# Performance work log

Measured on AMD Instinct MI355X. Metric: run time of the kernel, lower is better.

## Reference

```python
import jax, jax.numpy as jnp
import numpy as np

B, S, D = 2, 2048, 1024
H, KV, HD = 16, 4, 64
E, TOPK, F = 8, 2, 2048
EPS = 1e-5
THETA = 10000.0


def setup_inputs() -> dict:
    key = jax.random.key(0)
    ks = jax.random.split(key, 12)
    sc = 0.02
    x = jax.random.normal(ks[0], (B, S, D), jnp.float32)
    # real RoPE tables
    inv = 1.0 / (THETA ** (np.arange(0, HD, 2, dtype=np.float32) / HD))
    t = np.arange(S, dtype=np.float32)
    f = np.outer(t, inv)  # [S, HD/2]
    freqs_cos = jnp.asarray(np.cos(f), jnp.float32)
    freqs_sin = jnp.asarray(np.sin(f), jnp.float32)
    return {
        "x": x,
        "freqs_cos": freqs_cos,
        "freqs_sin": freqs_sin,
        "attn_norm_w": jnp.ones((D,), jnp.float32),
        "ffn_norm_w": jnp.ones((D,), jnp.float32),
        "wq": jax.random.normal(ks[1], (D, H * HD), jnp.float32) * sc,
        "wk": jax.random.normal(ks[2], (D, KV * HD), jnp.float32) * sc,
        "wv": jax.random.normal(ks[3], (D, KV * HD), jnp.float32) * sc,
        "wo": jax.random.normal(ks[4], (H * HD, D), jnp.float32) * sc,
        "gate_w": jax.random.normal(ks[5], (D, E), jnp.float32) * sc,
        "w1": jax.random.normal(ks[6], (E, D, F), jnp.float32) * sc,
        "w2": jax.random.normal(ks[7], (E, F, D), jnp.float32) * sc,
        "w3": jax.random.normal(ks[8], (E, D, F), jnp.float32) * sc,
    }


def rmsnorm(x, w):
    return x * jax.lax.rsqrt(jnp.mean(x * x, axis=-1, keepdims=True) + EPS) * w


def apply_rope(xq, cos, sin):
    # xq: [B,S,h,HD]; cos/sin: [S, HD/2]
    xr, xi = xq[..., 0::2], xq[..., 1::2]
    c = cos[None, :, None, :]
    s = sin[None, :, None, :]
    out = jnp.stack([xr * c - xi * s, xr * s + xi * c], axis=-1)
    return out.reshape(xq.shape)


def attention(xn, freqs_cos, freqs_sin, wq, wk, wv, wo):
    q = (xn @ wq).reshape(B, S, H, HD)
    k = (xn @ wk).reshape(B, S, KV, HD)
    v = (xn @ wv).reshape(B, S, KV, HD)
    q = apply_rope(q, freqs_cos, freqs_sin)
    k = apply_rope(k, freqs_cos, freqs_sin)
    n_rep = H // KV
    k = jnp.repeat(k, n_rep, axis=2)  # [B,S,H,HD]
    v = jnp.repeat(v, n_rep, axis=2)
    scores = jnp.einsum("bqhd,bkhd->bhqk", q, k) / jnp.sqrt(jnp.float32(HD))
    causal = jnp.tril(jnp.ones((S, S), bool))
    scores = jnp.where(causal[None, None], scores, jnp.finfo(scores.dtype).min)
    probs = jax.nn.softmax(scores, axis=-1)
    out = jnp.einsum("bhqk,bkhd->bqhd", probs, v).reshape(B, S, H * HD)
    return out @ wo


def sparse_moe(hn, gate_w, w1, w2, w3):
    xf = hn.reshape(-1, D)  # [T, D]
    probs = jax.nn.softmax(xf @ gate_w, axis=-1)  # [T, E]
    topv, topi = jax.lax.top_k(probs, TOPK)
    topv = topv / jnp.sum(topv, axis=-1, keepdims=True)
    # dense [T, E] routing weights (0 for non-selected experts)
    wdense = jnp.sum(jax.nn.one_hot(topi, E, dtype=xf.dtype) * topv[..., None], axis=1)
    h1 = jax.nn.silu(jnp.einsum("td,edf->etf", xf, w1))
    h3 = jnp.einsum("td,edf->etf", xf, w3)
    y = jnp.einsum("etf,efd->etd", h1 * h3, w2)
    out = jnp.einsum("te,etd->td", wdense, y)
    return out.reshape(B, S, D)


def reference(x, freqs_cos, freqs_sin, attn_norm_w, ffn_norm_w,
              wq, wk, wv, wo, gate_w, w1, w2, w3):
    h = x + attention(rmsnorm(x, attn_norm_w), freqs_cos, freqs_sin, wq, wk, wv, wo)
    out = h + sparse_moe(rmsnorm(h, ffn_norm_w), gate_w, w1, w2, w3)
    return out
```

## Files before the change

### kernel.cpp

```cpp
#include <hip/hip_runtime.h>
#include <stdint.h>

typedef unsigned short u16;
typedef unsigned int u32;
typedef __attribute__((ext_vector_type(8))) short short8;
typedef __attribute__((ext_vector_type(8))) u16 us8;
typedef __attribute__((ext_vector_type(4))) u16 us4;
typedef __attribute__((ext_vector_type(4))) float f32x4;

constexpr int NB = 2;
constexpr int SEQ = 2048;
constexpr int DIM = 1024;
constexpr int NH = 16;
constexpr int HD = 64;
constexpr int NE = 8;
constexpr int FF = 2048;
constexpr int TOK = NB * SEQ;
constexpr int NQKV = 1536;
constexpr int NPAIR = TOK * 2;
constexpr float REPS = 1e-5f;

#define VMCNT(n) asm volatile("s_waitcnt vmcnt(" #n ")" ::: "memory")
#define LGKM0 asm volatile("s_waitcnt lgkmcnt(0)" ::: "memory")

__device__ __forceinline__ u16 f2bf(float x) {
  union { float f; u32 u; } v; v.f = x;
  u32 r = v.u + 0x7fffu + ((v.u >> 16) & 1u);
  return (u16)(r >> 16);
}
__device__ __forceinline__ float bf2f(u16 h) {
  union { u32 u; float f; } v; v.u = ((u32)h) << 16;
  return v.f;
}

__device__ __forceinline__ void gl_lds16(const u16* g, u16* l) {
  __builtin_amdgcn_global_load_lds(
      (const __attribute__((address_space(1))) void*)g,
      (__attribute__((address_space(3))) void*)l, 16, 0, 0);
}

template <bool SPLIT>
__global__ __launch_bounds__(256) void tcvt_k(const float* __restrict__ src,
                                              u16* __restrict__ dhi,
                                              u16* __restrict__ dlo,
                                              int K, int N) {
  int z = blockIdx.z;
  src += (size_t)z * K * N;
  dhi += (size_t)z * K * N;
  if (SPLIT) dlo += (size_t)z * K * N;
  int n0 = blockIdx.x * 64, k0 = blockIdx.y * 64;
  __shared__ float tile[64][65];
  int t = threadIdx.x;
  int kk = t >> 4, nn4 = (t & 15) * 4;
#pragma unroll
  for (int i = 0; i < 4; i++) {
    int k = kk + i * 16;
    const float* p = src + (size_t)(k0 + k) * N + n0 + nn4;
    float4 v = *(const float4*)p;
    tile[nn4 + 0][k] = v.x;
    tile[nn4 + 1][k] = v.y;
    tile[nn4 + 2][k] = v.z;
    tile[nn4 + 3][k] = v.w;
  }
  __syncthreads();
  int nn = t >> 4, k4 = (t & 15) * 4;
#pragma unroll
  for (int i = 0; i < 4; i++) {
    int n = nn + i * 16;
    us4 hi, lo;
#pragma unroll
    for (int j = 0; j < 4; j++) {
      float f = tile[n][k4 + j];
      u16 h = f2bf(f);
      hi[j] = h;
      if (SPLIT) lo[j] = f2bf(f - bf2f(h));
    }
    *(us4*)(dhi + (size_t)(n0 + n) * K + k0 + k4) = hi;
    if (SPLIT) *(us4*)(dlo + (size_t)(n0 + n) * K + k0 + k4) = lo;
  }
}

template <bool SPLIT>
__global__ __launch_bounds__(256) void rmsnorm_k(const float* __restrict__ x,
                                                 const float* __restrict__ w,
                                                 u16* __restrict__ ohi,
                                                 u16* __restrict__ olo) {
  int row = blockIdx.x, t = threadIdx.x;
  float4 v = *(const float4*)(x + (size_t)row * DIM + t * 4);
  float ss = v.x * v.x + v.y * v.y + v.z * v.z + v.w * v.w;
#pragma unroll
  for (int m = 1; m < 64; m <<= 1) ss += __shfl_xor(ss, m);
  __shared__ float red[4];
  if ((t & 63) == 0) red[t >> 6] = ss;
  __syncthreads();
  float rstd = rsqrtf((red[0] + red[1] + red[2] + red[3]) * (1.0f / DIM) + REPS);
  float4 wv = *(const float4*)(w + t * 4);
  float os[4] = {v.x * rstd * wv.x, v.y * rstd * wv.y, v.z * rstd * wv.z,
                 v.w * rstd * wv.w};
  us4 hi, lo;
#pragma unroll
  for (int j = 0; j < 4; j++) {
    u16 h = f2bf(os[j]);
    hi[j] = h;
    if (SPLIT) lo[j] = f2bf(os[j] - bf2f(h));
  }
  *(us4*)(ohi + (size_t)row * DIM + t * 4) = hi;
  if (SPLIT) *(us4*)(olo + (size_t)row * DIM + t * 4) = lo;
}

template <int EPI, bool SPLIT, bool DUAL, bool PERSIST, int NXL, int NT>
__global__ __launch_bounds__(256, 2) void gemm_k(
    const u16* __restrict__ Ah, const u16* __restrict__ Al,
    const u16* __restrict__ Bh, const u16* __restrict__ Bl,
    const u16* __restrict__ B1, int N, int ldc,
    float* __restrict__ Cf, u16* __restrict__ Cb, float* __restrict__ C2,
    const float* __restrict__ resid, const int* __restrict__ cnt,
    const int* __restrict__ pids, const float* __restrict__ pw,
    const int* __restrict__ plan) {
  constexpr int K = NT * 32;
  constexpr int BN = SPLIT ? 64 : 128;
  constexpr int WCOL = BN / 2;
  constexpr int FN = BN / 32;
  constexpr int NAI = 2;
  constexpr int NBI = BN / 64;
  constexpr int BUFA = 128 * 32;
  constexpr int BUFB = BN * 32;
  constexpr bool L6 = SPLIT || DUAL;

  int tid = threadIdx.x, lane = tid & 63, wid = tid >> 6;
  int wm = wid >> 1, wn = wid & 1;
  int rr = lane & 15, g = lane >> 4;

  __shared__ u16 sAh[3 * BUFA];
  __shared__ u16 sAl[SPLIT ? 3 * BUFA : 16];
  __shared__ u16 sBh[3 * BUFB];
  __shared__ u16 sBl[SPLIT ? 3 * BUFB : 16];
  __shared__ u16 sB1[DUAL ? 3 * BUFB : 16];
  __shared__ int spid[PERSIST ? 128 : 8];
  __shared__ int srow[PERSIST ? 128 : 8];

  int pl[9];
  int items;
  if (PERSIST) {
#pragma unroll
    for (int e = 0; e < 9; e++) pl[e] = plan[e];
    items = pl[8] << NXL;
  } else {
    items = 1;
  }

  int it0 = PERSIST ? blockIdx.x : 0;
  int itstep = PERSIST ? gridDim.x : 1;
  for (int w = it0; w < items; w += itstep) {
    int m0, n0, z, cntz;
    if (PERSIST) {
      int wy = w >> NXL;
      int x = w & ((1 << NXL) - 1);
      z = 0;
#pragma unroll
      for (int e = 1; e < 8; e++) z += (wy >= pl[e]) ? 1 : 0;
      int yt = wy - pl[z];
      m0 = yt * 128;
      n0 = x * BN;
      cntz = cnt[z];
      if (tid < 128) {
        int i = m0 + tid;
        if (i > cntz - 1) i = cntz - 1;
        int p = pids[z * NPAIR + i];
        spid[tid] = p;
        srow[tid] = (EPI == 2) ? (p >> 1) : p;
      }
      __syncthreads();
    } else {
      m0 = blockIdx.y * 128;
      n0 = blockIdx.x * BN;
      z = 0;
      cntz = 1 << 30;
    }

    const u16* Bhz = Bh + (size_t)z * N * K;
    const u16* Blz = SPLIT ? Bl + (size_t)z * N * K : nullptr;
    const u16* B1z = DUAL ? B1 + (size_t)z * N * K : nullptr;

    int p4 = lane & 3;
    const u16 *agh[NAI], *agl[NAI];
    int aoff[NAI];
#pragma unroll
    for (int i = 0; i < NAI; i++) {
      int rl = i * 64 + wid * 16 + (lane >> 2);
      int gr = PERSIST ? srow[rl] : (m0 + rl);
      int sc = p4 ^ (rl & 3);
      agh[i] = Ah + (size_t)gr * K + sc * 8;
      if (SPLIT) agl[i] = Al + (size_t)gr * K + sc * 8;
      aoff[i] = (i * 4 + wid) * 512;
    }
    const u16 *bgh[NBI], *bgl[NBI], *bg1[NBI];
    int boff[NBI];
#pragma unroll
    for (int i = 0; i < NBI; i++) {
      int rl = i * 64 + wid * 16 + (lane >> 2);
      int sc = p4 ^ (rl & 3);
      size_t gr = (size_t)(n0 + rl) * K + sc * 8;
      bgh[i] = Bhz + gr;
      if (SPLIT) bgl[i] = Blz + gr;
      if (DUAL) bg1[i] = B1z + gr;
      boff[i] = (i * 4 + wid) * 512;
    }

    auto STAGE = [&](int kt, int bi) {
      int k0 = kt * 32;
#pragma unroll
      for (int i = 0; i < NAI; i++) {
        gl_lds16(agh[i] + k0, sAh + bi * BUFA + aoff[i]);
        if (SPLIT) gl_lds16(agl[i] + k0, sAl + bi * BUFA + aoff[i]);
      }
#pragma unroll
      for (int i = 0; i < NBI; i++) {
        gl_lds16(bgh[i] + k0, sBh + bi * BUFB + boff[i]);
        if (SPLIT) gl_lds16(bgl[i] + k0, sBl + bi * BUFB + boff[i]);
        if (DUAL) gl_lds16(bg1[i] + k0, sB1 + bi * BUFB + boff[i]);
      }
    };

    f32x4 zv = {0.f, 0.f, 0.f, 0.f};
    f32x4 acc[4][FN];
    f32x4 acc1[DUAL ? 4 : 1][DUAL ? FN : 1];
#pragma unroll
    for (int a = 0; a < 4; a++)
#pragma unroll
      for (int b = 0; b < FN; b++) {
        acc[a][b] = zv;
        if (DUAL) acc1[a][b] = zv;
      }

    STAGE(0, 0);
    STAGE(1, 1);
    STAGE(2, 2);

    int bi = 0;
    for (int t = 0; t < NT; t++) {
      int og = NT - 1 - t;
      if (L6) {
        if (og >= 2) VMCNT(12);
        else if (og == 1) VMCNT(6);
        else VMCNT(0);
      } else {
        if (og >= 2) VMCNT(8);
        else if (og == 1) VMCNT(4);
        else VMCNT(0);
      }
      __builtin_amdgcn_s_barrier();

      const u16* bA = sAh + bi * BUFA;
      const u16* bAl = sAl + (SPLIT ? bi * BUFA : 0);
      const u16* bB = sBh + bi * BUFB;
      const u16* bBl = sBl + (SPLIT ? bi * BUFB : 0);
      const u16* bB1 = sB1 + (DUAL ? bi * BUFB : 0);

      short8 a_h[4], a_l[4], b_h[FN], b_l[FN], b1f[FN];
#pragma unroll
      for (int f = 0; f < 4; f++) {
        int ra = wm * 64 + f * 16 + rr;
        int off = ra * 32 + ((g ^ (ra & 3)) * 8);
        a_h[f] = *(const short8*)&bA[off];
        if (SPLIT) a_l[f] = *(const short8*)&bAl[off];
      }
#pragma unroll
      for (int f = 0; f < FN; f++) {
        int rb = wn * WCOL + f * 16 + rr;
        int off = rb * 32 + ((g ^ (rb & 3)) * 8);
        b_h[f] = *(const short8*)&bB[off];
        if (SPLIT) b_l[f] = *(const short8*)&bBl[off];
        if (DUAL) b1f[f] = *(const short8*)&bB1[off];
      }
#pragma unroll
      for (int fm = 0; fm < 4; fm++)
#pragma unroll
        for (int fn = 0; fn < FN; fn++) {
          acc[fm][fn] = __builtin_amdgcn_mfma_f32_16x16x32_bf16(
              a_h[fm], b_h[fn], acc[fm][fn], 0, 0, 0);
          if (SPLIT) {
            acc[fm][fn] = __builtin_amdgcn_mfma_f32_16x16x32_bf16(
                a_h[fm], b_l[fn], acc[fm][fn], 0, 0, 0);
            acc[fm][fn] = __builtin_amdgcn_mfma_f32_16x16x32_bf16(
                a_l[fm], b_h[fn], acc[fm][fn], 0, 0, 0);
          }
          if (DUAL)
            acc1[fm][fn] = __builtin_amdgcn_mfma_f32_16x16x32_bf16(
                a_h[fm], b1f[fn], acc1[fm][fn], 0, 0, 0);
        }

      LGKM0;
      __builtin_amdgcn_s_barrier();
      if (t + 3 < NT) STAGE(t + 3, bi);
      bi = (bi == 2) ? 0 : bi + 1;
    }

#pragma unroll
    for (int fm = 0; fm < 4; fm++)
#pragma unroll
      for (int fn = 0; fn < FN; fn++)
#pragma unroll
        for (int rg = 0; rg < 4; rg++) {
          int rl = wm * 64 + fm * 16 + g * 4 + rg;
          int col = n0 + wn * WCOL + fn * 16 + rr;
          float v = acc[fm][fn][rg];
          if (EPI == 0) {
            Cf[(size_t)(m0 + rl) * ldc + col] = v;
          } else if (EPI == 1) {
            size_t idx = (size_t)(m0 + rl) * ldc + col;
            float r2 = v + resid[idx];
            Cf[idx] = r2;
            C2[idx] = r2;
          } else if (EPI == 2) {
            if (m0 + rl < cntz) {
              float gg = v / (1.0f + __expf(-v));
              float o = gg * acc1[fm][fn][rg];
              Cb[(size_t)spid[rl] * ldc + col] = f2bf(o);
            }
          } else {
            if (m0 + rl < cntz) {
              int p = spid[rl];
              atomicAdd(&Cf[(size_t)(p >> 1) * ldc + col], pw[p] * v);
            }
          }
        }
    if (PERSIST) __syncthreads();
  }
}

__global__ __launch_bounds__(256) void rope_k(float* __restrict__ qkv,
                                              const float* __restrict__ fc,
                                              const float* __restrict__ fs) {
  int idx = blockIdx.x * 256 + threadIdx.x;
  int i = idx & 31;
  int hh = (idx >> 5) % 20;
  int t = idx / 640;
  if (t >= TOK) return;
  int s = t & (SEQ - 1);
  int base = (hh < 16) ? (hh * 64) : (1024 + (hh - 16) * 64);
  float c = fc[s * 32 + i], sn = fs[s * 32 + i];
  float* p = qkv + (size_t)t * NQKV + base + 2 * i;
  float xr = p[0], xi = p[1];
  p[0] = xr * c - xi * sn;
  p[1] = xr * sn + xi * c;
}

__global__ __launch_bounds__(256) void cvtkv_k(const float* __restrict__ qkv,
                                               u16* __restrict__ Kh,
                                               u16* __restrict__ Kl,
                                               u16* __restrict__ Vh,
                                               u16* __restrict__ Vl) {
  int kvt = blockIdx.x;
  int kvh = blockIdx.y;
  int b = blockIdx.z;
  int t = threadIdx.x;
  __shared__ float vt[64][65];
  size_t tile = ((size_t)((b * 4 + kvh) * 32 + kvt)) * 4096;
  int r = t >> 2, c4 = t & 3;
  {
    const float* kp = qkv + ((size_t)(b * SEQ + kvt * 64 + r)) * NQKV + 1024 +
                      kvh * 64 + c4 * 16;
    float ff[16];
#pragma unroll
    for (int q = 0; q < 4; q++) {
      float4 f = *(const float4*)(kp + q * 4);
      ff[q * 4 + 0] = f.x; ff[q * 4 + 1] = f.y;
      ff[q * 4 + 2] = f.z; ff[q * 4 + 3] = f.w;
    }
#pragma unroll
    for (int half = 0; half < 2; half++) {
      int c = c4 * 2 + half;
      us8 hi, lo;
#pragma unroll
      for (int j = 0; j < 8; j++) {
        float f = ff[half * 8 + j];
        u16 h = f2bf(f);
        hi[j] = h;
        lo[j] = f2bf(f - bf2f(h));
      }
      int off = r * 64 + ((c ^ (r & 7)) * 8);
      *(us8*)(Kh + tile + off) = hi;
      *(us8*)(Kl + tile + off) = lo;
    }
  }
  {
    const float* vp = qkv + ((size_t)(b * SEQ + kvt * 64 + r)) * NQKV + 1280 +
                      kvh * 64 + c4 * 16;
#pragma unroll
    for (int q = 0; q < 4; q++) {
      float4 f = *(const float4*)(vp + q * 4);
      vt[r][c4 * 16 + q * 4 + 0] = f.x;
      vt[r][c4 * 16 + q * 4 + 1] = f.y;
      vt[r][c4 * 16 + q * 4 + 2] = f.z;
      vt[r][c4 * 16 + q * 4 + 3] = f.w;
    }
  }
  __syncthreads();
  {
    int d = t >> 2, g4 = t & 3;
    float ff[16];
#pragma unroll
    for (int j = 0; j < 16; j++) ff[j] = vt[g4 * 16 + j][d];
#pragma unroll
    for (int half = 0; half < 2; half++) {
      int c = g4 * 2 + half;
      us8 hi, lo;
#pragma unroll
      for (int j = 0; j < 8; j++) {
        float f = ff[half * 8 + j];
        u16 h = f2bf(f);
        hi[j] = h;
        lo[j] = f2bf(f - bf2f(h));
      }
      int off = d * 64 + ((c ^ (d & 7)) * 8);
      *(us8*)(Vh + tile + off) = hi;
      *(us8*)(Vl + tile + off) = lo;
    }
  }
}

__global__ __launch_bounds__(256, 2) void flash_k(
    const float* __restrict__ qkv, const u16* __restrict__ Kg,
    const u16* __restrict__ Klg, const u16* __restrict__ Vg,
    const u16* __restrict__ Vlg, u16* __restrict__ ah, u16* __restrict__ al) {
  int pi = blockIdx.x;
  int h = blockIdx.y;
  int b = blockIdx.z;
  int qt[2] = {31 - pi, pi};
  int kvh = h >> 2;
  int tid = threadIdx.x, lane = tid & 63, wid = tid >> 6;
  int rr = lane & 15, g = lane >> 4;

  __shared__ u16 sKh[4096], sKl[4096], sVh[4096], sVl[4096];
  __shared__ u32 sP[4][1024];

  f32x4 zv = {0.f, 0.f, 0.f, 0.f};
  short8 aqh[2][2], aql[2][2];
#pragma unroll
  for (int u = 0; u < 2; u++) {
    int qrow = qt[u] * 64 + wid * 16 + rr;
    const float* qp =
        qkv + ((size_t)(b * SEQ + qrow)) * NQKV + h * 64 + g * 8;
#pragma unroll
    for (int kc = 0; kc < 2; kc++) {
      float4 f0 = *(const float4*)(qp + kc * 32);
      float4 f1 = *(const float4*)(qp + kc * 32 + 4);
      float ff[8] = {f0.x, f0.y, f0.z, f0.w, f1.x, f1.y, f1.z, f1.w};
#pragma unroll
      for (int j = 0; j < 8; j++) {
        u16 hi = f2bf(ff[j]);
        aqh[u][kc][j] = (short)hi;
        aql[u][kc][j] = (short)f2bf(ff[j] - bf2f(hi));
      }
    }
  }

  f32x4 o[2][4];
  float m_r[2][4], l_r[2][4];
#pragma unroll
  for (int u = 0; u < 2; u++)
#pragma unroll
    for (int i = 0; i < 4; i++) {
      o[u][i] = zv;
      m_r[u][i] = -3.0e38f;
      l_r[u][i] = 0.f;
    }

  size_t tb = ((size_t)(b * 4 + kvh) * 32) * 4096;
  int so = tid * 16;
  us8 rKh[2], rKl[2], rVh[2], rVl[2];
  {
    size_t go = tb + so;
    rKh[0] = *(const us8*)(Kg + go);  rKh[1] = *(const us8*)(Kg + go + 8);
    rKl[0] = *(const us8*)(Klg + go); rKl[1] = *(const us8*)(Klg + go + 8);
    rVh[0] = *(const us8*)(Vg + go);  rVh[1] = *(const us8*)(Vg + go + 8);
    rVl[0] = *(const us8*)(Vlg + go); rVl[1] = *(const us8*)(Vlg + go + 8);
  }

  int nt = qt[0];
  for (int kvt = 0; kvt <= nt; kvt++) {
    __syncthreads();
    *(us8*)&sKh[so] = rKh[0]; *(us8*)&sKh[so + 8] = rKh[1];
    *(us8*)&sKl[so] = rKl[0]; *(us8*)&sKl[so + 8] = rKl[1];
    *(us8*)&sVh[so] = rVh[0]; *(us8*)&sVh[so + 8] = rVh[1];
    *(us8*)&sVl[so] = rVl[0]; *(us8*)&sVl[so + 8] = rVl[1];
    if (kvt < nt) {
      size_t go = tb + (size_t)(kvt + 1) * 4096 + so;
      rKh[0] = *(const us8*)(Kg + go);  rKh[1] = *(const us8*)(Kg + go + 8);
      rKl[0] = *(const us8*)(Klg + go); rKl[1] = *(const us8*)(Klg + go + 8);
      rVh[0] = *(const us8*)(Vg + go);  rVh[1] = *(const us8*)(Vg + go + 8);
      rVl[0] = *(const us8*)(Vlg + go); rVl[1] = *(const us8*)(Vlg + go + 8);
    }
    __syncthreads();

#pragma unroll
    for (int u = 0; u < 2; u++) {
      if (!(u == 1 && kvt > qt[1])) {
        float pv[4][4];
#pragma unroll
        for (int c16 = 0; c16 < 4; c16++) {
          int rk = c16 * 16 + rr;
          f32x4 sacc = zv;
#pragma unroll
          for (int kc = 0; kc < 2; kc++) {
            int sw = rk * 64 + (((kc * 4 + g) ^ (rk & 7)) * 8);
            short8 bh = *(const short8*)&sKh[sw];
            short8 bl = *(const short8*)&sKl[sw];
            sacc = __builtin_amdgcn_mfma_f32_16x16x32_bf16(aqh[u][kc], bh,
                                                           sacc, 0, 0, 0);
            sacc = __builtin_amdgcn_mfma_f32_16x16x32_bf16(aqh[u][kc], bl,
                                                           sacc, 0, 0, 0);
            sacc = __builtin_amdgcn_mfma_f32_16x16x32_bf16(aql[u][kc], bh,
                                                           sacc, 0, 0, 0);
          }
          bool diag = (kvt == qt[u]);
#pragma unroll
          for (int rg = 0; rg < 4; rg++) {
            float val = sacc[rg] * 0.125f;
            if (diag) {
              int kv_l = c16 * 16 + rr;
              int q_l = wid * 16 + g * 4 + rg;
              if (kv_l > q_l) val = -3.0e38f;
            }
            pv[c16][rg] = val;
          }
        }
        float pm[4];
#pragma unroll
        for (int rg = 0; rg < 4; rg++)
          pm[rg] = fmaxf(fmaxf(pv[0][rg], pv[1][rg]),
                         fmaxf(pv[2][rg], pv[3][rg]));
#pragma unroll
        for (int m = 1; m < 16; m <<= 1)
#pragma unroll
          for (int rg = 0; rg < 4; rg++)
            pm[rg] = fmaxf(pm[rg], __shfl_xor(pm[rg], m));
        float scl[4];
#pragma unroll
        for (int rg = 0; rg < 4; rg++) {
          float mn = fmaxf(m_r[u][rg], pm[rg]);
          scl[rg] = __expf(m_r[u][rg] - mn);
          m_r[u][rg] = mn;
        }
#pragma unroll
        for (int c16 = 0; c16 < 4; c16++)
#pragma unroll
          for (int rg = 0; rg < 4; rg++)
            pv[c16][rg] = __expf(pv[c16][rg] - m_r[u][rg]);
        float rsum[4];
#pragma unroll
        for (int rg = 0; rg < 4; rg++)
          rsum[rg] = pv[0][rg] + pv[1][rg] + pv[2][rg] + pv[3][rg];
#pragma unroll
        for (int m = 1; m < 16; m <<= 1)
#pragma unroll
          for (int rg = 0; rg < 4; rg++) rsum[rg] += __shfl_xor(rsum[rg], m);
#pragma unroll
        for (int rg = 0; rg < 4; rg++)
          l_r[u][rg] = l_r[u][rg] * scl[rg] + rsum[rg];
#pragma unroll
        for (int d16 = 0; d16 < 4; d16++)
#pragma unroll
          for (int rg = 0; rg < 4; rg++) o[u][d16][rg] *= scl[rg];

#pragma unroll
        for (int c16 = 0; c16 < 4; c16++)
#pragma unroll
          for (int rg = 0; rg < 4; rg++) {
            int ql = g * 4 + rg;
            int kvl = c16 * 16 + rr;
            u16 hi = f2bf(pv[c16][rg]);
            u16 lo = f2bf(pv[c16][rg] - bf2f(hi));
            sP[wid][ql * 64 + (kvl ^ (((ql >> 2) & 3) << 4))] =
                ((u32)lo << 16) | (u32)hi;
          }
        short8 pah[2], pal[2];
#pragma unroll
        for (int kc = 0; kc < 2; kc++) {
          int xb = (kc * 32 + g * 8) ^ (((rr >> 2) & 3) << 4);
          const u32* pp = &sP[wid][rr * 64 + xb];
#pragma unroll
          for (int j = 0; j < 8; j++) {
            u32 w = pp[j];
            pah[kc][j] = (short)(w & 0xffffu);
            pal[kc][j] = (short)(w >> 16);
          }
        }
#pragma unroll
        for (int d16 = 0; d16 < 4; d16++) {
          int rv = d16 * 16 + rr;
#pragma unroll
          for (int kc = 0; kc < 2; kc++) {
            int sw = rv * 64 + (((kc * 4 + g) ^ (rv & 7)) * 8);
            short8 vh = *(const short8*)&sVh[sw];
            short8 vl = *(const short8*)&sVl[sw];
            o[u][d16] = __builtin_amdgcn_mfma_f32_16x16x32_bf16(
                pah[kc], vh, o[u][d16], 0, 0, 0);
            o[u][d16] = __builtin_amdgcn_mfma_f32_16x16x32_bf16(
                pah[kc], vl, o[u][d16], 0, 0, 0);
            o[u][d16] = __builtin_amdgcn_mfma_f32_16x16x32_bf16(
                pal[kc], vh, o[u][d16], 0, 0, 0);
          }
        }
      }
    }
  }

#pragma unroll
  for (int u = 0; u < 2; u++)
#pragma unroll
    for (int rg = 0; rg < 4; rg++) {
      float inv = 1.0f / l_r[u][rg];
      int qr = qt[u] * 64 + wid * 16 + g * 4 + rg;
      size_t obase = (size_t)(b * SEQ + qr) * 1024 + h * 64;
#pragma unroll
      for (int d16 = 0; d16 < 4; d16++) {
        float v = o[u][d16][rg] * inv;
        u16 hi = f2bf(v);
        ah[obase + d16 * 16 + rr] = hi;
        al[obase + d16 * 16 + rr] = f2bf(v - bf2f(hi));
      }
    }
}

__global__ __launch_bounds__(256) void route_k(const float* __restrict__ h,
                                               const float* __restrict__ wffn,
                                               const float* __restrict__ gw,
                                               int* __restrict__ cnt,
                                               int* __restrict__ pids,
                                               float* __restrict__ pw) {
  int t = blockIdx.x, tid = threadIdx.x;
  float4 v = *(const float4*)(h + (size_t)t * DIM + tid * 4);
  float ss = v.x * v.x + v.y * v.y + v.z * v.z + v.w * v.w;
#pragma unroll
  for (int m = 1; m < 64; m <<= 1) ss += __shfl_xor(ss, m);
  __shared__ float red[4];
  if ((tid & 63) == 0) red[tid >> 6] = ss;
  __syncthreads();
  float rstd = rsqrtf((red[0] + red[1] + red[2] + red[3]) * (1.0f / DIM) + REPS);
  float4 wv = *(const float4*)(wffn + tid * 4);
  float xn[4] = {v.x * rstd * wv.x, v.y * rstd * wv.y, v.z * rstd * wv.z,
                 v.w * rstd * wv.w};
  float pl[8] = {0, 0, 0, 0, 0, 0, 0, 0};
#pragma unroll
  for (int j = 0; j < 4; j++) {
    const float* gp = gw + (size_t)(tid * 4 + j) * 8;
    float4 g0 = *(const float4*)gp;
    float4 g1 = *(const float4*)(gp + 4);
    pl[0] += xn[j] * g0.x; pl[1] += xn[j] * g0.y;
    pl[2] += xn[j] * g0.z; pl[3] += xn[j] * g0.w;
    pl[4] += xn[j] * g1.x; pl[5] += xn[j] * g1.y;
    pl[6] += xn[j] * g1.z; pl[7] += xn[j] * g1.w;
  }
#pragma unroll
  for (int e = 0; e < 8; e++)
#pragma unroll
    for (int m = 1; m < 64; m <<= 1) pl[e] += __shfl_xor(pl[e], m);
  __shared__ float lred[4][8];
  if ((tid & 63) == 0)
#pragma unroll
    for (int e = 0; e < 8; e++) lred[tid >> 6][e] = pl[e];
  __syncthreads();
  if (tid == 0) {
    float lg[8];
#pragma unroll
    for (int e = 0; e < 8; e++)
      lg[e] = lred[0][e] + lred[1][e] + lred[2][e] + lred[3][e];
    int e1 = 0;
    float l1 = lg[0];
#pragma unroll
    for (int e = 1; e < 8; e++)
      if (lg[e] > l1) { l1 = lg[e]; e1 = e; }
    int e2 = -1;
    float l2 = -3.0e38f;
#pragma unroll
    for (int e = 0; e < 8; e++)
      if (e != e1 && lg[e] > l2) { l2 = lg[e]; e2 = e; }
    float w1 = 1.0f / (1.0f + expf(l2 - l1));
    float w2 = 1.0f / (1.0f + expf(l1 - l2));
    int p0 = atomicAdd(&cnt[e1], 1);
    pids[e1 * NPAIR + p0] = t * 2;
    pw[t * 2] = w1;
    int p1 = atomicAdd(&cnt[e2], 1);
    pids[e2 * NPAIR + p1] = t * 2 + 1;
    pw[t * 2 + 1] = w2;
  }
}

__global__ void zero_k(int* cnt) {
  if (threadIdx.x < 8) cnt[threadIdx.x] = 0;
}

__global__ void plan_k(const int* __restrict__ cnt, int* __restrict__ plan) {
  if (threadIdx.x == 0) {
    int acc = 0;
    for (int e = 0; e < 8; e++) {
      plan[e] = acc;
      acc += (cnt[e] + 127) >> 7;
    }
    plan[8] = acc;
  }
}

extern "C" void kernel_launch(void* const* d_in, const int* in_sizes, int n_in,
                              void* d_out, int out_size, void* d_ws,
                              size_t ws_size, hipStream_t stream) {
  (void)in_sizes; (void)n_in; (void)out_size; (void)ws_size;
  const float* x = (const float*)d_in[0];
  const float* fc = (const float*)d_in[1];
  const float* fs = (const float*)d_in[2];
  const float* anw = (const float*)d_in[3];
  const float* fnw = (const float*)d_in[4];
  const float* wq = (const float*)d_in[5];
  const float* wk = (const float*)d_in[6];
  const float* wv = (const float*)d_in[7];
  const float* wo = (const float*)d_in[8];
  const float* gw = (const float*)d_in[9];
  const float* w1 = (const float*)d_in[10];
  const float* w2 = (const float*)d_in[11];
  const float* w3 = (const float*)d_in[12];
  float* outf = (float*)d_out;

  char* ws = (char*)d_ws;
  size_t off = 0;
  auto alloc = [&](size_t bytes) {
    void* p = ws + off;
    off += (bytes + 255) & ~(size_t)255;
    return p;
  };
  u16* wqkvT_h = (u16*)alloc((size_t)NQKV * DIM * 2);
  u16* wqkvT_l = (u16*)alloc((size_t)NQKV * DIM * 2);
  u16* woT_h = (u16*)alloc((size_t)DIM * DIM * 2);
  u16* woT_l = (u16*)alloc((size_t)DIM * DIM * 2);
  u16* w1T = (u16*)alloc((size_t)NE * FF * DIM * 2);
  u16* w3T = (u16*)alloc((size_t)NE * FF * DIM * 2);
  u16* w2T = (u16*)alloc((size_t)NE * DIM * FF * 2);
  u16* xnh = (u16*)alloc((size_t)TOK * DIM * 2);
  u16* xnl = (u16*)alloc((size_t)TOK * DIM * 2);
  float* qkvf = (float*)alloc((size_t)TOK * NQKV * 4);
  u16* attnh = (u16*)alloc((size_t)TOK * DIM * 2);
  u16* attnl = (u16*)alloc((size_t)TOK * DIM * 2);
  float* hbuf = (float*)alloc((size_t)TOK * DIM * 4);
  u16* hn = (u16*)alloc((size_t)TOK * DIM * 2);
  u16* h13 = (u16*)alloc((size_t)NPAIR * FF * 2);
  int* cnt = (int*)alloc(64);
  int* plan = (int*)alloc(64);
  int* pids = (int*)alloc((size_t)NE * NPAIR * 4);
  float* pwbuf = (float*)alloc((size_t)NPAIR * 4);
  u16* Ksw_h = (u16*)alloc((size_t)NB * 4 * SEQ * 64 * 2);
  u16* Ksw_l = (u16*)alloc((size_t)NB * 4 * SEQ * 64 * 2);
  u16* Vsw_h = (u16*)alloc((size_t)NB * 4 * SEQ * 64 * 2);
  u16* Vsw_l = (u16*)alloc((size_t)NB * 4 * SEQ * 64 * 2);

  dim3 blk(256);
  hipLaunchKernelGGL((tcvt_k<true>), dim3(16, 16, 1), blk, 0, stream, wq,
                     wqkvT_h, wqkvT_l, 1024, 1024);
  hipLaunchKernelGGL((tcvt_k<true>), dim3(4, 16, 1), blk, 0, stream, wk,
                     wqkvT_h + 1024 * 1024, wqkvT_l + 1024 * 1024, 1024, 256);
  hipLaunchKernelGGL((tcvt_k<true>), dim3(4, 16, 1), blk, 0, stream, wv,
                     wqkvT_h + 1280 * 1024, wqkvT_l + 1280 * 1024, 1024, 256);
  hipLaunchKernelGGL((tcvt_k<true>), dim3(16, 16, 1), blk, 0, stream, wo, woT_h,
                     woT_l, 1024, 1024);
  hipLaunchKernelGGL((tcvt_k<false>), dim3(32, 16, 8), blk, 0, stream, w1, w1T,
                     (u16*)nullptr, 1024, 2048);
  hipLaunchKernelGGL((tcvt_k<false>), dim3(32, 16, 8), blk, 0, stream, w3, w3T,
                     (u16*)nullptr, 1024, 2048);
  hipLaunchKernelGGL((tcvt_k<false>), dim3(16, 32, 8), blk, 0, stream, w2, w2T,
                     (u16*)nullptr, 2048, 1024);
  hipLaunchKernelGGL((rmsnorm_k<true>), dim3(TOK), blk, 0, stream, x, anw, xnh,
                     xnl);
  hipLaunchKernelGGL((gemm_k<0, true, false, false, 0, 32>),
                     dim3(NQKV / 64, TOK / 128, 1), blk, 0, stream, xnh, xnl,
                     wqkvT_h, wqkvT_l, (const u16*)nullptr, NQKV, NQKV, qkvf,
                     (u16*)nullptr, (float*)nullptr, (const float*)nullptr,
                     (const int*)nullptr, (const int*)nullptr,
                     (const float*)nullptr, (const int*)nullptr);
  hipLaunchKernelGGL(rope_k, dim3((TOK * 20 * 32) / 256), blk, 0, stream, qkvf,
                     fc, fs);
  hipLaunchKernelGGL(cvtkv_k, dim3(SEQ / 64, 4, NB), blk, 0, stream, qkvf,
                     Ksw_h, Ksw_l, Vsw_h, Vsw_l);
  hipLaunchKernelGGL(flash_k, dim3(16, NH, NB), blk, 0, stream, qkvf, Ksw_h,
                     Ksw_l, Vsw_h, Vsw_l, attnh, attnl);
  hipLaunchKernelGGL((gemm_k<1, true, false, false, 0, 32>),
                     dim3(DIM / 64, TOK / 128, 1), blk, 0, stream, attnh, attnl,
                     woT_h, woT_l, (const u16*)nullptr, DIM, DIM, hbuf,
                     (u16*)nullptr, outf, x, (const int*)nullptr,
                     (const int*)nullptr, (const float*)nullptr,
                     (const int*)nullptr);
  hipLaunchKernelGGL((rmsnorm_k<false>), dim3(TOK), blk, 0, stream, hbuf, fnw,
                     hn, (u16*)nullptr);
  hipLaunchKernelGGL(zero_k, dim3(1), dim3(64), 0, stream, cnt);
  hipLaunchKernelGGL(route_k, dim3(TOK), blk, 0, stream, hbuf, fnw, gw, cnt,
                     pids, pwbuf);
  hipLaunchKernelGGL(plan_k, dim3(1), dim3(64), 0, stream, cnt, plan);
  hipLaunchKernelGGL((gemm_k<2, false, true, true, 4, 32>), dim3(1024), blk, 0,
                     stream, hn, (const u16*)nullptr, w1T, (const u16*)nullptr,
                     w3T, FF, FF, (float*)nullptr, h13, (float*)nullptr,
                     (const float*)nullptr, cnt, pids, pwbuf, plan);
  hipLaunchKernelGGL((gemm_k<3, false, false, true, 3, 64>), dim3(1024), blk, 0,
                     stream, h13, (const u16*)nullptr, w2T, (const u16*)nullptr,
                     (const u16*)nullptr, DIM, DIM, outf, (u16*)nullptr,
                     (float*)nullptr, (const float*)nullptr, cnt, pids, pwbuf,
                     plan);
}
```

Before: 626.8 us.

## Load GEMM fragments directly from global into registers, dropping LDS staging

Replaces the triple-buffered global-to-LDS staging in the GEMM kernel with per-wave direct global loads into registers, double-buffered in registers across k-steps. This removes the LDS buffers, the vmcnt waits and the block barriers in the k-loop. The dual (w1/w3) GEMM is narrowed to 64-column tiles, with twice as many column tiles, to limit register pressure. The cost is that waves no longer share staged tiles, so each wave refetches its A and B fragments through the caches with smaller, less coalesced loads.

Result: slower. 978.9 us (+56.2%).

```diff
diff --git a/kernel.cpp b/kernel.cpp
--- a/kernel.cpp
+++ b/kernel.cpp
@@ -20,9 +20,6 @@
 constexpr int NPAIR = TOK * 2;
 constexpr float REPS = 1e-5f;
 
-#define VMCNT(n) asm volatile("s_waitcnt vmcnt(" #n ")" ::: "memory")
-#define LGKM0 asm volatile("s_waitcnt lgkmcnt(0)" ::: "memory")
-
 __device__ __forceinline__ u16 f2bf(float x) {
   union { float f; u32 u; } v; v.f = x;
   u32 r = v.u + 0x7fffu + ((v.u >> 16) & 1u);
@@ -31,12 +28,6 @@
 __device__ __forceinline__ float bf2f(u16 h) {
   union { u32 u; float f; } v; v.u = ((u32)h) << 16;
   return v.f;
-}
-
-__device__ __forceinline__ void gl_lds16(const u16* g, u16* l) {
-  __builtin_amdgcn_global_load_lds(
-      (const __attribute__((address_space(1))) void*)g,
-      (__attribute__((address_space(3))) void*)l, 16, 0, 0);
 }
 
 template <bool SPLIT>
@@ -108,6 +99,44 @@
   if (SPLIT) *(us4*)(olo + (size_t)row * DIM + t * 4) = lo;
 }
 
+#define LOADSET(S, kt)                                                       \
+  {                                                                          \
+    int ko = (kt)*32;                                                        \
+    _Pragma("unroll") for (int f = 0; f < 4; f++) A##S[f] =                  \
+        *(const short8*)(aP[f] + ko);                                        \
+    if constexpr (SPLIT) {                                                   \
+      _Pragma("unroll") for (int f = 0; f < 4; f++) AL##S[f] =               \
+          *(const short8*)(aPl[f] + ko);                                     \
+    }                                                                        \
+    _Pragma("unroll") for (int f = 0; f < FN; f++) B##S[f] =                 \
+        *(const short8*)(bP[f] + ko);                                        \
+    if constexpr (SPLIT) {                                                   \
+      _Pragma("unroll") for (int f = 0; f < FN; f++) BL##S[f] =              \
+          *(const short8*)(bPl[f] + ko);                                     \
+    }                                                                        \
+    if constexpr (DUAL) {                                                    \
+      _Pragma("unroll") for (int f = 0; f < FN; f++) D##S[f] =               \
+          *(const short8*)(b1P[f] + ko);                                     \
+    }                                                                        \
+  }
+
+#define MFMASET(S)                                                           \
+  _Pragma("unroll") for (int fm = 0; fm < 4; fm++) {                         \
+    _Pragma("unroll") for (int fn = 0; fn < FN; fn++) {                      \
+      acc[fm][fn] = __builtin_amdgcn_mfma_f32_16x16x32_bf16(                 \
+          A##S[fm], B##S[fn], acc[fm][fn], 0, 0, 0);                         \
+      if constexpr (SPLIT) {                                                 \
+        acc[fm][fn] = __builtin_amdgcn_mfma_f32_16x16x32_bf16(               \
+            A##S[fm], BL##S[fn], acc[fm][fn], 0, 0, 0);                      \
+        acc[fm][fn] = __builtin_amdgcn_mfma_f32_16x16x32_bf16(               \
+            AL##S[fm], B##S[fn], acc[fm][fn], 0, 0, 0);                      \
+      }                                                                      \
+      if constexpr (DUAL) acc1[fm][fn] =                                     \
+          __builtin_amdgcn_mfma_f32_16x16x32_bf16(A##S[fm], D##S[fn],        \
+                                                  acc1[fm][fn], 0, 0, 0);    \
+    }                                                                        \
+  }
+
 template <int EPI, bool SPLIT, bool DUAL, bool PERSIST, int NXL, int NT>
 __global__ __launch_bounds__(256, 2) void gemm_k(
     const u16* __restrict__ Ah, const u16* __restrict__ Al,
@@ -118,24 +147,14 @@
     const int* __restrict__ pids, const float* __restrict__ pw,
     const int* __restrict__ plan) {
   constexpr int K = NT * 32;
-  constexpr int BN = SPLIT ? 64 : 128;
+  constexpr int BN = (SPLIT || DUAL) ? 64 : 128;
   constexpr int WCOL = BN / 2;
-  constexpr int FN = BN / 32;
-  constexpr int NAI = 2;
-  constexpr int NBI = BN / 64;
-  constexpr int BUFA = 128 * 32;
-  constexpr int BUFB = BN * 32;
-  constexpr bool L6 = SPLIT || DUAL;
+  constexpr int FN = WCOL / 16;
 
   int tid = threadIdx.x, lane = tid & 63, wid = tid >> 6;
   int wm = wid >> 1, wn = wid & 1;
   int rr = lane & 15, g = lane >> 4;
 
-  __shared__ u16 sAh[3 * BUFA];
-  __shared__ u16 sAl[SPLIT ? 3 * BUFA : 16];
-  __shared__ u16 sBh[3 * BUFB];
-  __shared__ u16 sBl[SPLIT ? 3 * BUFB : 16];
-  __shared__ u16 sB1[DUAL ? 3 * BUFB : 16];
   __shared__ int spid[PERSIST ? 128 : 8];
   __shared__ int srow[PERSIST ? 128 : 8];
 
@@ -163,6 +182,7 @@
       m0 = yt * 128;
       n0 = x * BN;
       cntz = cnt[z];
+      __syncthreads();
       if (tid < 128) {
         int i = m0 + tid;
         if (i > cntz - 1) i = cntz - 1;
@@ -182,45 +202,22 @@
     const u16* Blz = SPLIT ? Bl + (size_t)z * N * K : nullptr;
     const u16* B1z = DUAL ? B1 + (size_t)z * N * K : nullptr;
 
-    int p4 = lane & 3;
-    const u16 *agh[NAI], *agl[NAI];
-    int aoff[NAI];
-#pragma unroll
-    for (int i = 0; i < NAI; i++) {
-      int rl = i * 64 + wid * 16 + (lane >> 2);
-      int gr = PERSIST ? srow[rl] : (m0 + rl);
-      int sc = p4 ^ (rl & 3);
-      agh[i] = Ah + (size_t)gr * K + sc * 8;
-      if (SPLIT) agl[i] = Al + (size_t)gr * K + sc * 8;
-      aoff[i] = (i * 4 + wid) * 512;
-    }
-    const u16 *bgh[NBI], *bgl[NBI], *bg1[NBI];
-    int boff[NBI];
-#pragma unroll
-    for (int i = 0; i < NBI; i++) {
-      int rl = i * 64 + wid * 16 + (lane >> 2);
-      int sc = p4 ^ (rl & 3);
-      size_t gr = (size_t)(n0 + rl) * K + sc * 8;
-      bgh[i] = Bhz + gr;
-      if (SPLIT) bgl[i] = Blz + gr;
-      if (DUAL) bg1[i] = B1z + gr;
-      boff[i] = (i * 4 + wid) * 512;
-    }
-
-    auto STAGE = [&](int kt, int bi) {
-      int k0 = kt * 32;
-#pragma unroll
-      for (int i = 0; i < NAI; i++) {
-        gl_lds16(agh[i] + k0, sAh + bi * BUFA + aoff[i]);
-        if (SPLIT) gl_lds16(agl[i] + k0, sAl + bi * BUFA + aoff[i]);
-      }
-#pragma unroll
-      for (int i = 0; i < NBI; i++) {
-        gl_lds16(bgh[i] + k0, sBh + bi * BUFB + boff[i]);
-        if (SPLIT) gl_lds16(bgl[i] + k0, sBl + bi * BUFB + boff[i]);
-        if (DUAL) gl_lds16(bg1[i] + k0, sB1 + bi * BUFB + boff[i]);
-      }
-    };
+    const u16 *aP[4], *aPl[SPLIT ? 4 : 1];
+#pragma unroll
+    for (int f = 0; f < 4; f++) {
+      int rl = wm * 64 + f * 16 + rr;
+      int ar = PERSIST ? srow[rl] : (m0 + rl);
+      aP[f] = Ah + (size_t)ar * K + g * 8;
+      if (SPLIT) aPl[f] = Al + (size_t)ar * K + g * 8;
+    }
+    const u16 *bP[FN], *bPl[SPLIT ? FN : 1], *b1P[DUAL ? FN : 1];
+#pragma unroll
+    for (int f = 0; f < FN; f++) {
+      size_t gr = (size_t)(n0 + wn * WCOL + f * 16 + rr) * K + g * 8;
+      bP[f] = Bhz + gr;
+      if (SPLIT) bPl[f] = Blz + gr;
+      if (DUAL) b1P[f] = B1z + gr;
+    }
 
     f32x4 zv = {0.f, 0.f, 0.f, 0.f};
     f32x4 acc[4][FN];
@@ -233,68 +230,21 @@
         if (DUAL) acc1[a][b] = zv;
       }
 
-    STAGE(0, 0);
-    STAGE(1, 1);
-    STAGE(2, 2);
-
-    int bi = 0;
-    for (int t = 0; t < NT; t++) {
-      int og = NT - 1 - t;
-      if (L6) {
-        if (og >= 2) VMCNT(12);
-        else if (og == 1) VMCNT(6);
-        else VMCNT(0);
-      } else {
-        if (og >= 2) VMCNT(8);
-        else if (og == 1) VMCNT(4);
-        else VMCNT(0);
-      }
-      __builtin_amdgcn_s_barrier();
-
-      const u16* bA = sAh + bi * BUFA;
-      const u16* bAl = sAl + (SPLIT ? bi * BUFA : 0);
-      const u16* bB = sBh + bi * BUFB;
-      const u16* bBl = sBl + (SPLIT ? bi * BUFB : 0);
-      const u16* bB1 = sB1 + (DUAL ? bi * BUFB : 0);
-
-      short8 a_h[4], a_l[4], b_h[FN], b_l[FN], b1f[FN];
-#pragma unroll
-      for (int f = 0; f < 4; f++) {
-        int ra = wm * 64 + f * 16 + rr;
-        int off = ra * 32 + ((g ^ (ra & 3)) * 8);
-        a_h[f] = *(const short8*)&bA[off];
-        if (SPLIT) a_l[f] = *(const short8*)&bAl[off];
-      }
-#pragma unroll
-      for (int f = 0; f < FN; f++) {
-        int rb = wn * WCOL + f * 16 + rr;
-        int off = rb * 32 + ((g ^ (rb & 3)) * 8);
-        b_h[f] = *(const short8*)&bB[off];
-        if (SPLIT) b_l[f] = *(const short8*)&bBl[off];
-        if (DUAL) b1f[f] = *(const short8*)&bB1[off];
-      }
-#pragma unroll
-      for (int fm = 0; fm < 4; fm++)
-#pragma unroll
-        for (int fn = 0; fn < FN; fn++) {
-          acc[fm][fn] = __builtin_amdgcn_mfma_f32_16x16x32_bf16(
-              a_h[fm], b_h[fn], acc[fm][fn], 0, 0, 0);
-          if (SPLIT) {
-            acc[fm][fn] = __builtin_amdgcn_mfma_f32_16x16x32_bf16(
-                a_h[fm], b_l[fn], acc[fm][fn], 0, 0, 0);
-            acc[fm][fn] = __builtin_amdgcn_mfma_f32_16x16x32_bf16(
-                a_l[fm], b_h[fn], acc[fm][fn], 0, 0, 0);
-          }
-          if (DUAL)
-            acc1[fm][fn] = __builtin_amdgcn_mfma_f32_16x16x32_bf16(
-                a_h[fm], b1f[fn], acc1[fm][fn], 0, 0, 0);
-        }
-
-      LGKM0;
-      __builtin_amdgcn_s_barrier();
-      if (t + 3 < NT) STAGE(t + 3, bi);
-      bi = (bi == 2) ? 0 : bi + 1;
-    }
+    short8 A0[4], A1[4];
+    short8 AL0[SPLIT ? 4 : 1], AL1[SPLIT ? 4 : 1];
+    short8 B0[FN], B1s[FN];
+    short8 BL0[SPLIT ? FN : 1], BL1[SPLIT ? FN : 1];
+    short8 D0[DUAL ? FN : 1], D1[DUAL ? FN : 1];
+#define B1 B1s
+    LOADSET(0, 0);
+#pragma unroll 1
+    for (int t = 0; t < NT; t += 2) {
+      LOADSET(1, t + 1);
+      MFMASET(0);
+      if (t + 2 < NT) LOADSET(0, t + 2);
+      MFMASET(1);
+    }
+#undef B1
 
 #pragma unroll
     for (int fm = 0; fm < 4; fm++)
@@ -325,7 +275,6 @@
             }
           }
         }
-    if (PERSIST) __syncthreads();
   }
 }
 
@@ -794,7 +743,7 @@
   hipLaunchKernelGGL(route_k, dim3(TOK), blk, 0, stream, hbuf, fnw, gw, cnt,
                      pids, pwbuf);
   hipLaunchKernelGGL(plan_k, dim3(1), dim3(64), 0, stream, cnt, plan);
-  hipLaunchKernelGGL((gemm_k<2, false, true, true, 4, 32>), dim3(1024), blk, 0,
+  hipLaunchKernelGGL((gemm_k<2, false, true, true, 5, 32>), dim3(1024), blk, 0,
                      stream, hn, (const u16*)nullptr, w1T, (const u16*)nullptr,
                      w3T, FF, FF, (float*)nullptr, h13, (float*)nullptr,
                      (const float*)nullptr, cnt, pids, pwbuf, plan);
```
